# Kernel tuning notes

Measured on AMD Instinct MI355X. Metric: run time of the kernel, lower is better.

The kernel has to match this reference:

```python
import jax, jax.numpy as jnp
import numpy as np

DIM = 512
HEADS = 8
HEAD_DIM = DIM // HEADS
SCALE = DIM ** (-0.5)  # note: original uses full dim, not head_dim


def setup_inputs() -> dict:
    key = jax.random.key(0)
    ks = jax.random.split(key, 7)
    B, N = 4, 2048
    x = jax.random.normal(ks[0], (B, N, DIM), dtype=jnp.float32)
    A_phi = jax.random.normal(ks[1], (B, N, N), dtype=jnp.float32)
    # parameters (torch Linear: y = x @ W.T + b)
    w_qkv = jax.random.normal(ks[2], (3 * DIM, DIM), dtype=jnp.float32) * (DIM ** -0.5)
    b_qkv = jax.random.normal(ks[3], (3 * DIM,), dtype=jnp.float32) * 0.02
    w_out = jax.random.normal(ks[4], (DIM, DIM), dtype=jnp.float32) * (DIM ** -0.5)
    b_out = jax.random.normal(ks[5], (DIM,), dtype=jnp.float32) * 0.02
    gamma = jnp.array(1.0, dtype=jnp.float32)
    return {"x": x, "A_phi": A_phi, "w_qkv": w_qkv, "b_qkv": b_qkv,
            "w_out": w_out, "b_out": b_out, "gamma": gamma}


def reference(x, A_phi, w_qkv, b_qkv, w_out, b_out, gamma):
    B, N, D = x.shape
    qkv = x @ w_qkv.T + b_qkv  # [B,N,3D]
    q, k, v = jnp.split(qkv, 3, axis=-1)
    def to_heads(t):
        return t.reshape(B, N, HEADS, HEAD_DIM).transpose(0, 2, 1, 3)  # [B,H,N,d]
    q, k, v = to_heads(q), to_heads(k), to_heads(v)
    attn = jnp.einsum('bhqd,bhkd->bhqk', q, k) * SCALE
    attn = attn + gamma * A_phi[:, None, :, :]
    attn = jax.nn.softmax(attn, axis=-1)
    out = jnp.einsum('bhqk,bhkd->bhqd', attn, v)
    out = out.transpose(0, 2, 1, 3).reshape(B, N, D)
    return out @ w_out.T + b_out
```

## Files before the change

kernel.cpp:

```cpp
#include <hip/hip_runtime.h>

#define NSEQ 2048
#define SCALE 0.04419417382415922f
#define LOG2E 1.44269504088896f

typedef __attribute__((ext_vector_type(8))) short short8v;
typedef __attribute__((ext_vector_type(4))) float f32x4;

#define GLOAD_LDS16(g, l) __builtin_amdgcn_global_load_lds( \
    (const __attribute__((address_space(1))) void*)(g),     \
    (__attribute__((address_space(3))) void*)(l), 16, 0, 0)

__device__ __forceinline__ unsigned short f2bf(float f) {
    unsigned int u = __builtin_bit_cast(unsigned int, f);
    u += 0x7fff + ((u >> 16) & 1);
    return (unsigned short)(u >> 16);
}

__device__ __forceinline__ float exp2_fast(float x) {
    float r; asm("v_exp_f32 %0, %1" : "=v"(r) : "v"(x)); return r;
}

__device__ __forceinline__ unsigned int pack_bf16_rh(float a, float b) {
    unsigned int ua = __builtin_bit_cast(unsigned int, a) + 0x8000u;
    unsigned int ub = __builtin_bit_cast(unsigned int, b) + 0x8000u;
    return __builtin_amdgcn_perm(ub, ua, 0x07060302u);
}

__global__ __launch_bounds__(256) void cvt_bf16(const float* __restrict__ in,
                                                unsigned short* __restrict__ out, int n4) {
    int i = blockIdx.x * 256 + threadIdx.x;
    if (i < n4) {
        float4 v = ((const float4*)in)[i];
        ushort4 o;
        o.x = f2bf(v.x); o.y = f2bf(v.y); o.z = f2bf(v.z); o.w = f2bf(v.w);
        ((ushort4*)out)[i] = o;
    }
}

template<int MODE>
__global__ __launch_bounds__(256) void gemm_bf16(
    const unsigned short* __restrict__ A,
    const unsigned short* __restrict__ W,
    const float* __restrict__ bias,
    unsigned short* __restrict__ Qws,
    unsigned short* __restrict__ Kws,
    unsigned short* __restrict__ Vtws,
    float* __restrict__ Cout)
{
    __shared__ __attribute__((aligned(16))) unsigned short As[128 * 64];
    __shared__ __attribute__((aligned(16))) unsigned short Bs[128 * 64];

    int tid = threadIdx.x;
    int lane = tid & 63, w = tid >> 6;
    int wm = w >> 1, wn = w & 1;
    int g = lane >> 4, fr = lane & 15;
    int m0 = blockIdx.y * 128, n0 = blockIdx.x * 128;

    f32x4 acc[4][4] = {};

    for (int k0 = 0; k0 < 512; k0 += 64) {
        __syncthreads();
#pragma unroll
        for (int c = 0; c < 4; ++c) {
            int chunk = tid + c * 256;
            int row = chunk >> 3, c8 = chunk & 7;
            int gcol = (c8 ^ (row & 7)) * 8;
            GLOAD_LDS16(A + (size_t)(m0 + row) * 512 + k0 + gcol, &As[chunk * 8]);
            GLOAD_LDS16(W + (size_t)(n0 + row) * 512 + k0 + gcol, &Bs[chunk * 8]);
        }
        __syncthreads();
#pragma unroll
        for (int kk = 0; kk < 2; ++kk) {
            short8v af[4], bf[4];
#pragma unroll
            for (int mi = 0; mi < 4; ++mi) {
                int row = wm * 64 + mi * 16 + fr;
                af[mi] = *(const short8v*)(&As[row * 64 + (((kk * 4 + g) ^ (row & 7)) * 8)]);
            }
#pragma unroll
            for (int ni = 0; ni < 4; ++ni) {
                int row = wn * 64 + ni * 16 + fr;
                bf[ni] = *(const short8v*)(&Bs[row * 64 + (((kk * 4 + g) ^ (row & 7)) * 8)]);
            }
#pragma unroll
            for (int mi = 0; mi < 4; ++mi)
#pragma unroll
                for (int ni = 0; ni < 4; ++ni)
                    acc[mi][ni] = __builtin_amdgcn_mfma_f32_16x16x32_bf16(
                        af[mi], bf[ni], acc[mi][ni], 0, 0, 0);
        }
    }

#pragma unroll
    for (int mi = 0; mi < 4; ++mi) {
#pragma unroll
        for (int ni = 0; ni < 4; ++ni) {
            int col = n0 + wn * 64 + ni * 16 + fr;
            float bb = bias[col];
#pragma unroll
            for (int r = 0; r < 4; ++r) {
                int row = m0 + wm * 64 + mi * 16 + g * 4 + r;
                float val = acc[mi][ni][r] + bb;
                if (MODE == 0) {
                    int b = row >> 11, s = row & 2047;
                    if (col < 512) {
                        int h = col >> 6, d = col & 63;
                        Qws[(((size_t)(b * 8 + h) * NSEQ + s) << 6) + d] = f2bf(val * (SCALE * LOG2E));
                    } else if (col < 1024) {
                        int c2 = col - 512; int h = c2 >> 6, d = c2 & 63;
                        Kws[(((size_t)(b * 8 + h) * NSEQ + s) << 6) + d] = f2bf(val);
                    } else {
                        int c2 = col - 1024; int h = c2 >> 6, d = c2 & 63;
                        Vtws[((size_t)(b * 8 + h) * 64 + d) * NSEQ + s] = f2bf(val);
                    }
                } else {
                    Cout[(size_t)row * 512 + col] = val;
                }
            }
        }
    }
}

__global__ __launch_bounds__(512, 3) void attn_kernel(
    const unsigned short* __restrict__ Qws,
    const unsigned short* __restrict__ Kws,
    const unsigned short* __restrict__ Vtws,
    const float* __restrict__ A_phi,
    const float* __restrict__ gamma_p,
    unsigned short* __restrict__ Oout)
{
    __shared__ __attribute__((aligned(16))) unsigned short Ks[2][64 * 64];
    __shared__ __attribute__((aligned(16))) unsigned short Vts[2][64 * 64];
    __shared__ __attribute__((aligned(16))) unsigned short Pl[8][16 * 64];

    int tid = threadIdx.x, lane = tid & 63, w = tid >> 6;
    int g = lane >> 4, fr = lane & 15;

    int id = blockIdx.x;
    int b = (id & 7) >> 1, p = id & 1;
    int j = id >> 3;
    int h = j & 7;
    int qt = ((j >> 3) << 1) | p;
    int bh = b * 8 + h;
    int q0 = qt * 128 + w * 16;
    float g2 = gamma_p[0] * LOG2E;

    const unsigned short* Kb = Kws + (size_t)bh * NSEQ * 64;
    const unsigned short* Vb = Vtws + (size_t)bh * 64 * NSEQ;
    const float* Ap = A_phi + (size_t)b * NSEQ * NSEQ;

    short8v qf[2];
#pragma unroll
    for (int dc = 0; dc < 2; ++dc)
        qf[dc] = *(const short8v*)(Qws + ((size_t)bh * NSEQ + q0 + fr) * 64 + dc * 32 + g * 8);

    int c = tid;
    int krow = c >> 3;
    int kchunk = c & 7;
    int swK = (kchunk ^ ((krow >> 2) & 7)) * 8;
    int swV = (kchunk ^ (krow & 7)) * 8;
    int kcol = kchunk * 8;

    float l_lane[4] = {};
    f32x4 o_acc[4] = {};

    {
        short8v k0v = *(const short8v*)(Kb + c * 8);
        short8v v0v = *(const short8v*)(Vb + (size_t)krow * NSEQ + kcol);
        *(short8v*)(&Ks[0][krow * 64 + swK]) = k0v;
        *(short8v*)(&Vts[0][krow * 64 + swV]) = v0v;
    }
    __syncthreads();

    for (int kt = 0; kt < NSEQ / 64; ++kt) {
        int cur = kt & 1;

        short8v kreg, vreg;
        if (kt < NSEQ / 64 - 1) {
            kreg = *(const short8v*)(Kb + (kt + 1) * 4096 + c * 8);
            vreg = *(const short8v*)(Vb + (size_t)krow * NSEQ + (kt + 1) * 64 + kcol);
        }

        float4 av[4];
#pragma unroll
        for (int r = 0; r < 4; ++r)
            av[r] = *(const float4*)(Ap + (size_t)(q0 + g * 4 + r) * NSEQ + kt * 64 + 4 * fr);

        f32x4 sa[4] = {};
        __builtin_amdgcn_s_setprio(1);
#pragma unroll
        for (int kf = 0; kf < 4; ++kf) {
            int row = 4 * fr + kf;
#pragma unroll
            for (int dc = 0; dc < 2; ++dc) {
                short8v kfrag = *(const short8v*)(
                    &Ks[cur][row * 64 + (((dc * 4 + g) ^ ((row >> 2) & 7)) * 8)]);
                sa[kf] = __builtin_amdgcn_mfma_f32_16x16x32_bf16(qf[dc], kfrag, sa[kf], 0, 0, 0);
            }
        }
        __builtin_amdgcn_s_setprio(0);

#pragma unroll
        for (int r = 0; r < 4; ++r) {
            float e0 = exp2_fast(fmaf(g2, av[r].x, sa[0][r]));
            float e1 = exp2_fast(fmaf(g2, av[r].y, sa[1][r]));
            float e2 = exp2_fast(fmaf(g2, av[r].z, sa[2][r]));
            float e3 = exp2_fast(fmaf(g2, av[r].w, sa[3][r]));
            l_lane[r] += (e0 + e1) + (e2 + e3);
            int rp = g * 4 + r;
            uint2 pp;
            pp.x = pack_bf16_rh(e0, e1);
            pp.y = pack_bf16_rh(e2, e3);
            *(uint2*)(&Pl[w][rp * 64 + (((fr >> 1) ^ (rp & 7)) * 8) + (fr & 1) * 4]) = pp;
        }
        asm volatile("s_waitcnt lgkmcnt(0)" ::: "memory");

#pragma unroll
        for (int kc = 0; kc < 2; ++kc) {
            short8v pf = *(const short8v*)(
                &Pl[w][fr * 64 + (((kc * 4 + g) ^ (fr & 7)) * 8)]);
            __builtin_amdgcn_s_setprio(1);
#pragma unroll
            for (int nf = 0; nf < 4; ++nf) {
                int vrow = nf * 16 + fr;
                short8v vf = *(const short8v*)(
                    &Vts[cur][vrow * 64 + (((kc * 4 + g) ^ (vrow & 7)) * 8)]);
                o_acc[nf] = __builtin_amdgcn_mfma_f32_16x16x32_bf16(pf, vf, o_acc[nf], 0, 0, 0);
            }
            __builtin_amdgcn_s_setprio(0);
        }

        if (kt < NSEQ / 64 - 1) {
            *(short8v*)(&Ks[cur ^ 1][krow * 64 + swK]) = kreg;
            *(short8v*)(&Vts[cur ^ 1][krow * 64 + swV]) = vreg;
        }
        __syncthreads();
    }

#pragma unroll
    for (int r = 0; r < 4; ++r) {
        float l = l_lane[r];
        l += __shfl_xor(l, 1);
        l += __shfl_xor(l, 2);
        l += __shfl_xor(l, 4);
        l += __shfl_xor(l, 8);
        float inv = 1.0f / l;
        int qg = q0 + g * 4 + r;
#pragma unroll
        for (int nf = 0; nf < 4; ++nf)
            Oout[((size_t)b * NSEQ + qg) * 512 + h * 64 + nf * 16 + fr] =
                f2bf(o_acc[nf][r] * inv);
    }
}

extern "C" void kernel_launch(void* const* d_in, const int* in_sizes, int n_in,
                              void* d_out, int out_size, void* d_ws, size_t ws_size,
                              hipStream_t stream) {
    const float* x      = (const float*)d_in[0];
    const float* A_phi  = (const float*)d_in[1];
    const float* w_qkv  = (const float*)d_in[2];
    const float* b_qkv  = (const float*)d_in[3];
    const float* w_out  = (const float*)d_in[4];
    const float* b_out  = (const float*)d_in[5];
    const float* gamma  = (const float*)d_in[6];
    float* out = (float*)d_out;

    unsigned short* xb   = (unsigned short*)d_ws;
    unsigned short* wqb  = xb  + (size_t)8192 * 512;
    unsigned short* wob  = wqb + (size_t)1536 * 512;
    unsigned short* Qws  = wob + (size_t)512 * 512;
    unsigned short* Kws  = Qws + (size_t)4 * 8 * NSEQ * 64;
    unsigned short* Vtws = Kws + (size_t)4 * 8 * NSEQ * 64;
    unsigned short* Oat  = Vtws + (size_t)4 * 8 * NSEQ * 64;

    cvt_bf16<<<dim3(4096), dim3(256), 0, stream>>>(x, xb, 8192 * 512 / 4);
    cvt_bf16<<<dim3(768),  dim3(256), 0, stream>>>(w_qkv, wqb, 1536 * 512 / 4);
    cvt_bf16<<<dim3(256),  dim3(256), 0, stream>>>(w_out, wob, 512 * 512 / 4);

    gemm_bf16<0><<<dim3(12, 64), dim3(256), 0, stream>>>(
        xb, wqb, b_qkv, Qws, Kws, Vtws, nullptr);

    attn_kernel<<<dim3(512), dim3(512), 0, stream>>>(
        Qws, Kws, Vtws, A_phi, gamma, Oat);

    gemm_bf16<1><<<dim3(4, 64), dim3(256), 0, stream>>>(
        Oat, wob, b_out, nullptr, nullptr, nullptr, out);
}
```

Before: 124.3 us.

## Load V fragments directly from global into registers, dropping LDS staging

The V^T tile is no longer staged through double-buffered shared memory. Each lane now loads its own MFMA B-operand fragments straight from global memory, issued after the QK^T MFMAs. This removes the LDS writes and reads for V and frees shared memory. In exchange, every wave re-reads V from global or cache with no reuse across the block's 8 waves, and the per-thread register count grows, so the launch bound is lowered from 3 to 2 blocks per CU.

```diff
diff --git a/kernel.cpp b/kernel.cpp
--- a/kernel.cpp
+++ b/kernel.cpp
@@ -122,7 +122,7 @@
     }
 }
 
-__global__ __launch_bounds__(512, 3) void attn_kernel(
+__global__ __launch_bounds__(512, 2) void attn_kernel(
     const unsigned short* __restrict__ Qws,
     const unsigned short* __restrict__ Kws,
     const unsigned short* __restrict__ Vtws,
@@ -131,7 +131,6 @@
     unsigned short* __restrict__ Oout)
 {
     __shared__ __attribute__((aligned(16))) unsigned short Ks[2][64 * 64];
-    __shared__ __attribute__((aligned(16))) unsigned short Vts[2][64 * 64];
     __shared__ __attribute__((aligned(16))) unsigned short Pl[8][16 * 64];
 
     int tid = threadIdx.x, lane = tid & 63, w = tid >> 6;
@@ -159,28 +158,24 @@
     int krow = c >> 3;
     int kchunk = c & 7;
     int swK = (kchunk ^ ((krow >> 2) & 7)) * 8;
-    int swV = (kchunk ^ (krow & 7)) * 8;
-    int kcol = kchunk * 8;
+
+    const unsigned short* Vlane = Vb + (size_t)fr * NSEQ + g * 8;
 
     float l_lane[4] = {};
     f32x4 o_acc[4] = {};
 
     {
         short8v k0v = *(const short8v*)(Kb + c * 8);
-        short8v v0v = *(const short8v*)(Vb + (size_t)krow * NSEQ + kcol);
         *(short8v*)(&Ks[0][krow * 64 + swK]) = k0v;
-        *(short8v*)(&Vts[0][krow * 64 + swV]) = v0v;
     }
     __syncthreads();
 
     for (int kt = 0; kt < NSEQ / 64; ++kt) {
         int cur = kt & 1;
 
-        short8v kreg, vreg;
-        if (kt < NSEQ / 64 - 1) {
+        short8v kreg;
+        if (kt < NSEQ / 64 - 1)
             kreg = *(const short8v*)(Kb + (kt + 1) * 4096 + c * 8);
-            vreg = *(const short8v*)(Vb + (size_t)krow * NSEQ + (kt + 1) * 64 + kcol);
-        }
 
         float4 av[4];
 #pragma unroll
@@ -200,6 +195,14 @@
             }
         }
         __builtin_amdgcn_s_setprio(0);
+
+        short8v vf[2][4];
+#pragma unroll
+        for (int kc = 0; kc < 2; ++kc)
+#pragma unroll
+            for (int nf = 0; nf < 4; ++nf)
+                vf[kc][nf] = *(const short8v*)(
+                    Vlane + (size_t)(nf * 16) * NSEQ + kt * 64 + kc * 32);
 
 #pragma unroll
         for (int r = 0; r < 4; ++r) {
@@ -222,19 +225,14 @@
                 &Pl[w][fr * 64 + (((kc * 4 + g) ^ (fr & 7)) * 8)]);
             __builtin_amdgcn_s_setprio(1);
 #pragma unroll
-            for (int nf = 0; nf < 4; ++nf) {
-                int vrow = nf * 16 + fr;
-                short8v vf = *(const short8v*)(
-                    &Vts[cur][vrow * 64 + (((kc * 4 + g) ^ (vrow & 7)) * 8)]);
-                o_acc[nf] = __builtin_amdgcn_mfma_f32_16x16x32_bf16(pf, vf, o_acc[nf], 0, 0, 0);
-            }
+            for (int nf = 0; nf < 4; ++nf)
+                o_acc[nf] = __builtin_amdgcn_mfma_f32_16x16x32_bf16(
+                    pf, vf[kc][nf], o_acc[nf], 0, 0, 0);
             __builtin_amdgcn_s_setprio(0);
         }
 
-        if (kt < NSEQ / 64 - 1) {
+        if (kt < NSEQ / 64 - 1)
             *(short8v*)(&Ks[cur ^ 1][krow * 64 + swK]) = kreg;
-            *(short8v*)(&Vts[cur ^ 1][krow * 64 + swV]) = vreg;
-        }
         __syncthreads();
     }
 
```

Result: slower. 210.0 us (+69.0%).
